# Kernel optimization log

Measured on AMD Instinct MI355X. Metric: run time of the kernel, lower is better.

The kernel has to match this reference:

```python
import jax, jax.numpy as jnp
import numpy as np

EMB = 512
N_ROWS = 10000
N_PAIRS = 65536


def setup_inputs() -> dict:
    key = jax.random.key(0)
    ks = jax.random.split(key, 10)
    s1 = 1.0 / np.sqrt(2 * EMB)
    s2 = 1.0 / np.sqrt(128)
    s3 = 1.0 / np.sqrt(64)
    return {
        "pos_pairs": jax.random.randint(ks[0], (N_PAIRS, 3), 0, N_ROWS, dtype=jnp.int32),
        "neg_pairs": jax.random.randint(ks[1], (N_PAIRS, 3), 0, N_ROWS, dtype=jnp.int32),
        "drug_embedding": jax.random.normal(ks[2], (N_ROWS, EMB), dtype=jnp.float32),
        "target_embedding": jax.random.normal(ks[3], (N_ROWS, EMB), dtype=jnp.float32),
        "W1": jax.random.normal(ks[4], (2 * EMB, 128), dtype=jnp.float32) * s1,
        "b1": jnp.zeros((128,), dtype=jnp.float32),
        "W2": jax.random.normal(ks[5], (128, 64), dtype=jnp.float32) * s2,
        "b2": jnp.zeros((64,), dtype=jnp.float32),
        "W3": jax.random.normal(ks[6], (64, 1), dtype=jnp.float32) * s3,
        "b3": jnp.zeros((1,), dtype=jnp.float32),
    }


def _mlp(x, W1, b1, W2, b2, W3, b3):
    h = jax.nn.relu(x @ W1 + b1)
    h = jax.nn.relu(h @ W2 + b2)
    return (h @ W3 + b3)[..., 0]  # [N]


def _pair_loss(pairs, drug_emb, tgt_emb, W1, b1, W2, b2, W3, b3):
    d = drug_emb[pairs[:, 0]]            # [N, EMB]
    t1 = tgt_emb[pairs[:, 1]]            # [N, EMB]
    t2 = tgt_emb[pairs[:, 2]]            # [N, EMB]
    a1 = _mlp(jnp.concatenate([d, t1], axis=-1), W1, b1, W2, b2, W3, b3)
    a2 = _mlp(jnp.concatenate([d, t2], axis=-1), W1, b1, W2, b2, W3, b3)
    # per-pair MSE of scalar affinities = (a1 - a2)^2; mean over pairs
    return jnp.mean((a1 - a2) ** 2)


def reference(pos_pairs, neg_pairs, drug_embedding, target_embedding,
              W1, b1, W2, b2, W3, b3):
    pos = _pair_loss(pos_pairs, drug_embedding, target_embedding, W1, b1, W2, b2, W3, b3)
    neg = _pair_loss(neg_pairs, drug_embedding, target_embedding, W1, b1, W2, b2, W3, b3)
    return pos - neg
```

## Files before the change

kernel.cpp:

```cpp
#include <hip/hip_runtime.h>

#define EMB 512
#define NROWS 10000
#define NPAIRS 65536

typedef __bf16 bf16x8 __attribute__((ext_vector_type(8)));
typedef float  f32x4  __attribute__((ext_vector_type(4)));
typedef unsigned int u32x4 __attribute__((ext_vector_type(4)));

__device__ __forceinline__ void split2(float x0, float x1, unsigned* hw, unsigned* lw) {
    unsigned u0 = __float_as_uint(x0), u1 = __float_as_uint(x1);
    unsigned r0 = u0 + 0x7FFFu + ((u0 >> 16) & 1u);
    unsigned r1 = u1 + 0x7FFFu + ((u1 >> 16) & 1u);
    float h0 = __uint_as_float(r0 & 0xFFFF0000u);
    float h1 = __uint_as_float(r1 & 0xFFFF0000u);
    float l0 = x0 - h0, l1 = x1 - h1;
    unsigned v0 = __float_as_uint(l0), v1 = __float_as_uint(l1);
    unsigned s0 = v0 + 0x7FFFu + ((v0 >> 16) & 1u);
    unsigned s1 = v1 + 0x7FFFu + ((v1 >> 16) & 1u);
    *hw = (r0 >> 16) | (r1 & 0xFFFF0000u);
    *lw = (s0 >> 16) | (s1 & 0xFFFF0000u);
}

__global__ __launch_bounds__(256)
void k0_fragment(const float* __restrict__ W1, const float* __restrict__ W2,
                 unsigned short* __restrict__ W1Fhi, unsigned short* __restrict__ W1Flo,
                 unsigned short* __restrict__ W2Fhi, unsigned short* __restrict__ W2Flo)
{
    int e = blockIdx.x * 256 + threadIdx.x;
    float x;
    unsigned short *hp, *lp;
    if (e < 131072) {
        int i  = e & 7;
        int l  = (e >> 3) & 63;
        int nt = (e >> 9) & 7;
        int kt = (e >> 12) & 15;
        int t  = e >> 16;
        int k = kt * 32 + 8 * (l >> 4) + i;
        int n = nt * 16 + (l & 15);
        x = W1[(t * 512 + k) * 128 + n];
        hp = W1Fhi + e; lp = W1Flo + e;
    } else {
        int e2 = e - 131072;
        int i  = e2 & 7;
        int l  = (e2 >> 3) & 63;
        int nt = (e2 >> 9) & 3;
        int kt = e2 >> 11;
        int k = kt * 32 + 8 * (l >> 4) + i;
        int n = nt * 16 + (l & 15);
        x = W2[k * 64 + n];
        hp = W2Fhi + e2; lp = W2Flo + e2;
    }
    unsigned u = __float_as_uint(x);
    unsigned r = u + 0x7FFFu + ((u >> 16) & 1u);
    float hf = __uint_as_float(r & 0xFFFF0000u);
    float lf = x - hf;
    unsigned v = __float_as_uint(lf);
    unsigned s = v + 0x7FFFu + ((v >> 16) & 1u);
    *hp = (unsigned short)(r >> 16);
    *lp = (unsigned short)(s >> 16);
}

#define K1_RT 313

__global__ __launch_bounds__(256)
void k1_mfma(const float* __restrict__ drug, const float* __restrict__ tgt,
             const unsigned* __restrict__ W1Fhi, const unsigned* __restrict__ W1Flo,
             const float* __restrict__ b1,
             float* __restrict__ D, float* __restrict__ T)
{
    __shared__ float Abuf[2][32 * 64];

    int bid = blockIdx.x, tid = threadIdx.x;
    bool isT = bid >= K1_RT;
    int rt = isT ? bid - K1_RT : bid;
    const float* emb = isT ? tgt : drug;
    float* out = isT ? T : D;
    int row0 = rt * 32;

    int wave = tid >> 6, lane = tid & 63;
    int g = lane >> 4, lm = lane & 15;
    int mt = wave & 1, nh = wave >> 1;

    int rr = lane >> 4, cc = lane & 15;
    const float* sp[2];
    #pragma unroll
    for (int it = 0; it < 2; it++) {
        int srow = row0 + wave * 8 + it * 4 + rr;
        if (srow > NROWS - 1) srow = NROWS - 1;
        int schunk = (cc & 8) | ((cc & 7) ^ (srow & 7));
        sp[it] = emb + (size_t)srow * EMB + schunk * 4;
    }

    const u32x4* BH = (const u32x4*)W1Fhi + (isT ? 8192 : 0);
    const u32x4* BL = (const u32x4*)W1Flo + (isT ? 8192 : 0);

    int r = mt * 16 + lm, rs = r & 7;

    f32x4 acc[4];
    #pragma unroll
    for (int j = 0; j < 4; j++) { acc[j][0]=0.f; acc[j][1]=0.f; acc[j][2]=0.f; acc[j][3]=0.f; }

    #pragma unroll
    for (int it = 0; it < 2; it++)
        __builtin_amdgcn_global_load_lds(
            (const __attribute__((address_space(1))) void*)(sp[it]),
            (__attribute__((address_space(3))) void*)((char*)&Abuf[0][0] + wave * 2048 + it * 1024),
            16, 0, 0);

    #pragma unroll
    for (int step = 0; step < 8; step++) {
        int cur = step & 1;
        u32x4 bh[2][4], bl[2][4];
        #pragma unroll
        for (int s = 0; s < 2; s++)
            #pragma unroll
            for (int j = 0; j < 4; j++) {
                int kt32 = step * 2 + s, nt = nh * 4 + j;
                bh[s][j] = BH[(kt32 * 8 + nt) * 64 + lane];
                bl[s][j] = BL[(kt32 * 8 + nt) * 64 + lane];
            }
        if (step < 7) {
            #pragma unroll
            for (int it = 0; it < 2; it++)
                __builtin_amdgcn_global_load_lds(
                    (const __attribute__((address_space(1))) void*)(sp[it] + (step + 1) * 64),
                    (__attribute__((address_space(3))) void*)((char*)&Abuf[cur ^ 1][0] + wave * 2048 + it * 1024),
                    16, 0, 0);
            asm volatile("s_waitcnt vmcnt(2)" ::: "memory");
        } else {
            asm volatile("s_waitcnt vmcnt(0)" ::: "memory");
        }
        __builtin_amdgcn_s_barrier();
        const f32x4* A4 = (const f32x4*)&Abuf[cur][0];
        #pragma unroll
        for (int s = 0; s < 2; s++) {
            f32x4 a0 = A4[r * 16 + s * 8 + ((2 * g) ^ rs)];
            f32x4 a1 = A4[r * 16 + s * 8 + ((2 * g + 1) ^ rs)];
            unsigned h0, h1, h2, h3, l0, l1, l2, l3;
            split2(a0[0], a0[1], &h0, &l0);
            split2(a0[2], a0[3], &h1, &l1);
            split2(a1[0], a1[1], &h2, &l2);
            split2(a1[2], a1[3], &h3, &l3);
            u32x4 ah, al;
            ah[0]=h0; ah[1]=h1; ah[2]=h2; ah[3]=h3;
            al[0]=l0; al[1]=l1; al[2]=l2; al[3]=l3;
            bf16x8 Ah = __builtin_bit_cast(bf16x8, ah);
            bf16x8 Al = __builtin_bit_cast(bf16x8, al);
            #pragma unroll
            for (int j = 0; j < 4; j++) {
                bf16x8 Bh = __builtin_bit_cast(bf16x8, bh[s][j]);
                bf16x8 Bl = __builtin_bit_cast(bf16x8, bl[s][j]);
                acc[j] = __builtin_amdgcn_mfma_f32_16x16x32_bf16(Ah, Bh, acc[j], 0, 0, 0);
                acc[j] = __builtin_amdgcn_mfma_f32_16x16x32_bf16(Ah, Bl, acc[j], 0, 0, 0);
                acc[j] = __builtin_amdgcn_mfma_f32_16x16x32_bf16(Al, Bh, acc[j], 0, 0, 0);
            }
        }
        asm volatile("s_waitcnt lgkmcnt(0)" ::: "memory");
        __builtin_amdgcn_s_barrier();
    }

    #pragma unroll
    for (int j = 0; j < 4; j++) {
        int col = (nh * 4 + j) * 16 + lm;
        float bias = isT ? 0.f : b1[col];
        #pragma unroll
        for (int reg = 0; reg < 4; reg++) {
            int row = row0 + mt * 16 + 4 * g + reg;
            if (row < NROWS) out[row * 128 + col] = acc[j][reg] + bias;
        }
    }
}

__global__ __launch_bounds__(256, 4)
void k2_pairs(const float* __restrict__ D, const float* __restrict__ T,
              const int* __restrict__ pos, const int* __restrict__ neg,
              const unsigned* __restrict__ W2Fhi, const unsigned* __restrict__ W2Flo,
              const float* __restrict__ b2, const float* __restrict__ W3,
              double* __restrict__ partials)
{
    __shared__ float Sbuf[2][96 * 32];
    __shared__ double red[4];

    int tid = threadIdx.x, bid = blockIdx.x;
    int wave = tid >> 6, lane = tid & 63;
    int g = lane >> 4, lm = lane & 15;
    const int* pairs = (bid < 2048) ? pos : neg;
    int p0 = (bid & 2047) * 32;

    int rr = lane >> 3, cc = lane & 7;
    const float* sp[3];
    #pragma unroll
    for (int it = 0; it < 3; it++) {
        int pr = wave * 24 + it * 8 + rr;
        int idxv;
        const float* src;
        if (pr < 32) { idxv = pairs[(p0 + pr) * 3]; src = D; }
        else { int q = pr - 32; idxv = pairs[(p0 + (q >> 1)) * 3 + 1 + (q & 1)]; src = T; }
        sp[it] = src + (size_t)idxv * 128 + ((cc ^ (pr & 7)) << 2);
    }

    const u32x4* BH4 = (const u32x4*)W2Fhi;
    const u32x4* BL4 = (const u32x4*)W2Flo;

    int mt = wave;
    int r = mt * 16 + lm;
    int p = r >> 1;
    int ds = p & 7, ts = r & 7;

    f32x4 acc[4];
    #pragma unroll
    for (int nt = 0; nt < 4; nt++) { acc[nt][0]=0.f; acc[nt][1]=0.f; acc[nt][2]=0.f; acc[nt][3]=0.f; }

    #pragma unroll
    for (int it = 0; it < 3; it++)
        __builtin_amdgcn_global_load_lds(
            (const __attribute__((address_space(1))) void*)(sp[it]),
            (__attribute__((address_space(3))) void*)((char*)&Sbuf[0][0] + wave * 3072 + it * 1024),
            16, 0, 0);

    #pragma unroll
    for (int step = 0; step < 4; step++) {
        int cur = step & 1;
        u32x4 bh[4], bl[4];
        #pragma unroll
        for (int nt = 0; nt < 4; nt++) {
            bh[nt] = BH4[(step * 4 + nt) * 64 + lane];
            bl[nt] = BL4[(step * 4 + nt) * 64 + lane];
        }
        if (step < 3) {
            #pragma unroll
            for (int it = 0; it < 3; it++)
                __builtin_amdgcn_global_load_lds(
                    (const __attribute__((address_space(1))) void*)(sp[it] + (step + 1) * 32),
                    (__attribute__((address_space(3))) void*)((char*)&Sbuf[cur ^ 1][0] + wave * 3072 + it * 1024),
                    16, 0, 0);
            asm volatile("s_waitcnt vmcnt(3)" ::: "memory");
        } else {
            asm volatile("s_waitcnt vmcnt(0)" ::: "memory");
        }
        __builtin_amdgcn_s_barrier();
        const f32x4* dS = (const f32x4*)&Sbuf[cur][0];
        f32x4 d0 = dS[p * 8 + ((2 * g) ^ ds)];
        f32x4 d1 = dS[p * 8 + ((2 * g + 1) ^ ds)];
        f32x4 t0 = dS[(32 + r) * 8 + ((2 * g) ^ ts)];
        f32x4 t1 = dS[(32 + r) * 8 + ((2 * g + 1) ^ ts)];
        float h0 = fmaxf(d0[0] + t0[0], 0.f), h1v = fmaxf(d0[1] + t0[1], 0.f);
        float h2 = fmaxf(d0[2] + t0[2], 0.f), h3 = fmaxf(d0[3] + t0[3], 0.f);
        float h4 = fmaxf(d1[0] + t1[0], 0.f), h5 = fmaxf(d1[1] + t1[1], 0.f);
        float h6 = fmaxf(d1[2] + t1[2], 0.f), h7 = fmaxf(d1[3] + t1[3], 0.f);
        unsigned hq0, hq1, hq2, hq3, lq0, lq1, lq2, lq3;
        split2(h0, h1v, &hq0, &lq0);
        split2(h2, h3,  &hq1, &lq1);
        split2(h4, h5,  &hq2, &lq2);
        split2(h6, h7,  &hq3, &lq3);
        u32x4 ah, al;
        ah[0]=hq0; ah[1]=hq1; ah[2]=hq2; ah[3]=hq3;
        al[0]=lq0; al[1]=lq1; al[2]=lq2; al[3]=lq3;
        bf16x8 Ah = __builtin_bit_cast(bf16x8, ah);
        bf16x8 Al = __builtin_bit_cast(bf16x8, al);
        #pragma unroll
        for (int nt = 0; nt < 4; nt++) {
            bf16x8 Bh = __builtin_bit_cast(bf16x8, bh[nt]);
            bf16x8 Bl = __builtin_bit_cast(bf16x8, bl[nt]);
            acc[nt] = __builtin_amdgcn_mfma_f32_16x16x32_bf16(Ah, Bh, acc[nt], 0, 0, 0);
            acc[nt] = __builtin_amdgcn_mfma_f32_16x16x32_bf16(Ah, Bl, acc[nt], 0, 0, 0);
            acc[nt] = __builtin_amdgcn_mfma_f32_16x16x32_bf16(Al, Bh, acc[nt], 0, 0, 0);
        }
        asm volatile("s_waitcnt lgkmcnt(0)" ::: "memory");
        __builtin_amdgcn_s_barrier();
    }

    float b2v[4], w3v[4];
    #pragma unroll
    for (int nt = 0; nt < 4; nt++) { b2v[nt] = b2[nt * 16 + lm]; w3v[nt] = W3[nt * 16 + lm]; }

    float pr[4];
    #pragma unroll
    for (int reg = 0; reg < 4; reg++) {
        float s = 0.f;
        #pragma unroll
        for (int nt = 0; nt < 4; nt++) {
            float h2 = fmaxf(acc[nt][reg] + b2v[nt], 0.f);
            s = fmaf(h2, w3v[nt], s);
        }
        pr[reg] = s;
    }
    #pragma unroll
    for (int m = 1; m <= 8; m <<= 1)
        #pragma unroll
        for (int reg = 0; reg < 4; reg++)
            pr[reg] += __shfl_xor(pr[reg], m, 64);

    float dd0 = pr[0] - pr[1];
    float dd1 = pr[2] - pr[3];
    double dsq = (double)dd0 * (double)dd0 + (double)dd1 * (double)dd1;
    dsq += __shfl_xor(dsq, 16, 64);
    dsq += __shfl_xor(dsq, 32, 64);

    if (lane == 0) red[wave] = dsq;
    __syncthreads();
    if (tid == 0) partials[bid] = red[0] + red[1] + red[2] + red[3];
}

__global__ __launch_bounds__(256)
void k3_final(const double* __restrict__ partials, float* __restrict__ out)
{
    __shared__ double sred[2][4];
    int t = threadIdx.x;
    double sp = 0.0, sn = 0.0;
    #pragma unroll
    for (int i = 0; i < 8; i++) {
        sp += partials[t + 256 * i];
        sn += partials[2048 + t + 256 * i];
    }
    #pragma unroll
    for (int m = 1; m <= 32; m <<= 1) {
        sp += __shfl_xor(sp, m, 64);
        sn += __shfl_xor(sn, m, 64);
    }
    int wave = t >> 6, lane = t & 63;
    if (lane == 0) { sred[0][wave] = sp; sred[1][wave] = sn; }
    __syncthreads();
    if (t == 0) {
        double SP = sred[0][0] + sred[0][1] + sred[0][2] + sred[0][3];
        double SN = sred[1][0] + sred[1][1] + sred[1][2] + sred[1][3];
        out[0] = (float)((SP - SN) / (double)NPAIRS);
    }
}

extern "C" void kernel_launch(void* const* d_in, const int* in_sizes, int n_in,
                              void* d_out, int out_size, void* d_ws, size_t ws_size,
                              hipStream_t stream) {
    const int*   pos  = (const int*)d_in[0];
    const int*   neg  = (const int*)d_in[1];
    const float* drug = (const float*)d_in[2];
    const float* tgt  = (const float*)d_in[3];
    const float* W1   = (const float*)d_in[4];
    const float* b1   = (const float*)d_in[5];
    const float* W2   = (const float*)d_in[6];
    const float* b2   = (const float*)d_in[7];
    const float* W3   = (const float*)d_in[8];

    float* Dp = (float*)d_ws;
    float* Tp = Dp + NROWS * 128;
    char* base = (char*)(Tp + NROWS * 128);
    unsigned short* W2Fhi = (unsigned short*)base;
    unsigned short* W2Flo = W2Fhi + 8192;
    unsigned short* W1Fhi = W2Flo + 8192;
    unsigned short* W1Flo = W1Fhi + 131072;
    double* partials = (double*)(W1Flo + 131072);
    float* out = (float*)d_out;

    k0_fragment<<<544, 256, 0, stream>>>(W1, W2, W1Fhi, W1Flo, W2Fhi, W2Flo);
    k1_mfma<<<2 * K1_RT, 256, 0, stream>>>(drug, tgt, (const unsigned*)W1Fhi,
                                           (const unsigned*)W1Flo, b1, Dp, Tp);
    k2_pairs<<<4096, 256, 0, stream>>>(Dp, Tp, pos, neg, (const unsigned*)W2Fhi,
                                       (const unsigned*)W2Flo, b2, W3, partials);
    k3_final<<<1, 256, 0, stream>>>(partials, out);
}
```

Baseline: 64.18 us.

## Load full K tile into LDS upfront, drop per-step double-buffer barriers

Both kernels now issue every global-to-LDS load for the whole K dimension at the start (64KB for k1, 48KB for k2), then run one barrier followed by a barrier-free MFMA loop. The aim is to remove the per-step waitcnt/barrier handshakes of the double-buffered pipeline and keep more loads in flight at once. The cost is much larger LDS per block, which lowers occupancy. Any overlap between loading and compute now has to come from other resident blocks. The launch bound hint of 4 blocks on k2 is removed to match.

```diff
diff --git a/kernel.cpp b/kernel.cpp
--- a/kernel.cpp
+++ b/kernel.cpp
@@ -69,7 +69,7 @@
              const float* __restrict__ b1,
              float* __restrict__ D, float* __restrict__ T)
 {
-    __shared__ float Abuf[2][32 * 64];
+    __shared__ float Abuf[32 * 512];
 
     int bid = blockIdx.x, tid = threadIdx.x;
     bool isT = bid >= K1_RT;
@@ -82,82 +82,59 @@
     int g = lane >> 4, lm = lane & 15;
     int mt = wave & 1, nh = wave >> 1;
 
-    int rr = lane >> 4, cc = lane & 15;
-    const float* sp[2];
-    #pragma unroll
-    for (int it = 0; it < 2; it++) {
-        int srow = row0 + wave * 8 + it * 4 + rr;
+    #pragma unroll
+    for (int it = 0; it < 16; it++) {
+        int pr = wave * 8 + (it >> 1);
+        int srow = row0 + pr;
         if (srow > NROWS - 1) srow = NROWS - 1;
-        int schunk = (cc & 8) | ((cc & 7) ^ (srow & 7));
-        sp[it] = emb + (size_t)srow * EMB + schunk * 4;
-    }
+        int c = (it & 1) * 64 + lane;
+        int sc = (c & ~7) | ((lane & 7) ^ (pr & 7));
+        __builtin_amdgcn_global_load_lds(
+            (const __attribute__((address_space(1))) void*)(emb + (size_t)srow * EMB + sc * 4),
+            (__attribute__((address_space(3))) void*)((char*)Abuf + wave * 16384 + it * 1024),
+            16, 0, 0);
+    }
+    __syncthreads();
 
     const u32x4* BH = (const u32x4*)W1Fhi + (isT ? 8192 : 0);
     const u32x4* BL = (const u32x4*)W1Flo + (isT ? 8192 : 0);
-
-    int r = mt * 16 + lm, rs = r & 7;
+    const f32x4* A4 = (const f32x4*)Abuf;
+
+    int r = mt * 16 + lm, rk = r & 7;
 
     f32x4 acc[4];
     #pragma unroll
     for (int j = 0; j < 4; j++) { acc[j][0]=0.f; acc[j][1]=0.f; acc[j][2]=0.f; acc[j][3]=0.f; }
 
-    #pragma unroll
-    for (int it = 0; it < 2; it++)
-        __builtin_amdgcn_global_load_lds(
-            (const __attribute__((address_space(1))) void*)(sp[it]),
-            (__attribute__((address_space(3))) void*)((char*)&Abuf[0][0] + wave * 2048 + it * 1024),
-            16, 0, 0);
-
-    #pragma unroll
-    for (int step = 0; step < 8; step++) {
-        int cur = step & 1;
-        u32x4 bh[2][4], bl[2][4];
-        #pragma unroll
-        for (int s = 0; s < 2; s++)
-            #pragma unroll
-            for (int j = 0; j < 4; j++) {
-                int kt32 = step * 2 + s, nt = nh * 4 + j;
-                bh[s][j] = BH[(kt32 * 8 + nt) * 64 + lane];
-                bl[s][j] = BL[(kt32 * 8 + nt) * 64 + lane];
-            }
-        if (step < 7) {
-            #pragma unroll
-            for (int it = 0; it < 2; it++)
-                __builtin_amdgcn_global_load_lds(
-                    (const __attribute__((address_space(1))) void*)(sp[it] + (step + 1) * 64),
-                    (__attribute__((address_space(3))) void*)((char*)&Abuf[cur ^ 1][0] + wave * 2048 + it * 1024),
-                    16, 0, 0);
-            asm volatile("s_waitcnt vmcnt(2)" ::: "memory");
-        } else {
-            asm volatile("s_waitcnt vmcnt(0)" ::: "memory");
-        }
-        __builtin_amdgcn_s_barrier();
-        const f32x4* A4 = (const f32x4*)&Abuf[cur][0];
-        #pragma unroll
-        for (int s = 0; s < 2; s++) {
-            f32x4 a0 = A4[r * 16 + s * 8 + ((2 * g) ^ rs)];
-            f32x4 a1 = A4[r * 16 + s * 8 + ((2 * g + 1) ^ rs)];
-            unsigned h0, h1, h2, h3, l0, l1, l2, l3;
-            split2(a0[0], a0[1], &h0, &l0);
-            split2(a0[2], a0[3], &h1, &l1);
-            split2(a1[0], a1[1], &h2, &l2);
-            split2(a1[2], a1[3], &h3, &l3);
-            u32x4 ah, al;
-            ah[0]=h0; ah[1]=h1; ah[2]=h2; ah[3]=h3;
-            al[0]=l0; al[1]=l1; al[2]=l2; al[3]=l3;
-            bf16x8 Ah = __builtin_bit_cast(bf16x8, ah);
-            bf16x8 Al = __builtin_bit_cast(bf16x8, al);
-            #pragma unroll
-            for (int j = 0; j < 4; j++) {
-                bf16x8 Bh = __builtin_bit_cast(bf16x8, bh[s][j]);
-                bf16x8 Bl = __builtin_bit_cast(bf16x8, bl[s][j]);
-                acc[j] = __builtin_amdgcn_mfma_f32_16x16x32_bf16(Ah, Bh, acc[j], 0, 0, 0);
-                acc[j] = __builtin_amdgcn_mfma_f32_16x16x32_bf16(Ah, Bl, acc[j], 0, 0, 0);
-                acc[j] = __builtin_amdgcn_mfma_f32_16x16x32_bf16(Al, Bh, acc[j], 0, 0, 0);
-            }
-        }
-        asm volatile("s_waitcnt lgkmcnt(0)" ::: "memory");
-        __builtin_amdgcn_s_barrier();
+    #pragma unroll 4
+    for (int kt = 0; kt < 16; kt++) {
+        u32x4 bh[4], bl[4];
+        #pragma unroll
+        for (int j = 0; j < 4; j++) {
+            int nt = nh * 4 + j;
+            bh[j] = BH[(kt * 8 + nt) * 64 + lane];
+            bl[j] = BL[(kt * 8 + nt) * 64 + lane];
+        }
+        f32x4 a0 = A4[r * 128 + kt * 8 + ((2 * g)     ^ rk)];
+        f32x4 a1 = A4[r * 128 + kt * 8 + ((2 * g + 1) ^ rk)];
+        unsigned h0, h1, h2, h3, l0, l1, l2, l3;
+        split2(a0[0], a0[1], &h0, &l0);
+        split2(a0[2], a0[3], &h1, &l1);
+        split2(a1[0], a1[1], &h2, &l2);
+        split2(a1[2], a1[3], &h3, &l3);
+        u32x4 ah, al;
+        ah[0]=h0; ah[1]=h1; ah[2]=h2; ah[3]=h3;
+        al[0]=l0; al[1]=l1; al[2]=l2; al[3]=l3;
+        bf16x8 Ah = __builtin_bit_cast(bf16x8, ah);
+        bf16x8 Al = __builtin_bit_cast(bf16x8, al);
+        #pragma unroll
+        for (int j = 0; j < 4; j++) {
+            bf16x8 Bh = __builtin_bit_cast(bf16x8, bh[j]);
+            bf16x8 Bl = __builtin_bit_cast(bf16x8, bl[j]);
+            acc[j] = __builtin_amdgcn_mfma_f32_16x16x32_bf16(Ah, Bh, acc[j], 0, 0, 0);
+            acc[j] = __builtin_amdgcn_mfma_f32_16x16x32_bf16(Ah, Bl, acc[j], 0, 0, 0);
+            acc[j] = __builtin_amdgcn_mfma_f32_16x16x32_bf16(Al, Bh, acc[j], 0, 0, 0);
+        }
     }
 
     #pragma unroll
@@ -172,14 +149,14 @@
     }
 }
 
-__global__ __launch_bounds__(256, 4)
+__global__ __launch_bounds__(256)
 void k2_pairs(const float* __restrict__ D, const float* __restrict__ T,
               const int* __restrict__ pos, const int* __restrict__ neg,
               const unsigned* __restrict__ W2Fhi, const unsigned* __restrict__ W2Flo,
               const float* __restrict__ b2, const float* __restrict__ W3,
               double* __restrict__ partials)
 {
-    __shared__ float Sbuf[2][96 * 32];
+    __shared__ float Sbuf[96 * 128];
     __shared__ double red[4];
 
     int tid = threadIdx.x, bid = blockIdx.x;
@@ -188,63 +165,46 @@
     const int* pairs = (bid < 2048) ? pos : neg;
     int p0 = (bid & 2047) * 32;
 
-    int rr = lane >> 3, cc = lane & 7;
-    const float* sp[3];
-    #pragma unroll
-    for (int it = 0; it < 3; it++) {
-        int pr = wave * 24 + it * 8 + rr;
+    #pragma unroll
+    for (int it = 0; it < 12; it++) {
+        int pr = wave * 24 + it * 2 + (lane >> 5);
         int idxv;
         const float* src;
         if (pr < 32) { idxv = pairs[(p0 + pr) * 3]; src = D; }
         else { int q = pr - 32; idxv = pairs[(p0 + (q >> 1)) * 3 + 1 + (q & 1)]; src = T; }
-        sp[it] = src + (size_t)idxv * 128 + ((cc ^ (pr & 7)) << 2);
-    }
+        int c = lane & 31;
+        int sc = (c & 24) | ((c & 7) ^ (pr & 7));
+        __builtin_amdgcn_global_load_lds(
+            (const __attribute__((address_space(1))) void*)(src + (size_t)idxv * 128 + sc * 4),
+            (__attribute__((address_space(3))) void*)((char*)Sbuf + wave * 12288 + it * 1024),
+            16, 0, 0);
+    }
+    __syncthreads();
 
     const u32x4* BH4 = (const u32x4*)W2Fhi;
     const u32x4* BL4 = (const u32x4*)W2Flo;
-
-    int mt = wave;
-    int r = mt * 16 + lm;
+    const f32x4* S4 = (const f32x4*)Sbuf;
+
+    int r = wave * 16 + lm;
     int p = r >> 1;
-    int ds = p & 7, ts = r & 7;
+    int pk = p & 7, tk = r & 7;
 
     f32x4 acc[4];
     #pragma unroll
     for (int nt = 0; nt < 4; nt++) { acc[nt][0]=0.f; acc[nt][1]=0.f; acc[nt][2]=0.f; acc[nt][3]=0.f; }
 
     #pragma unroll
-    for (int it = 0; it < 3; it++)
-        __builtin_amdgcn_global_load_lds(
-            (const __attribute__((address_space(1))) void*)(sp[it]),
-            (__attribute__((address_space(3))) void*)((char*)&Sbuf[0][0] + wave * 3072 + it * 1024),
-            16, 0, 0);
-
-    #pragma unroll
     for (int step = 0; step < 4; step++) {
-        int cur = step & 1;
         u32x4 bh[4], bl[4];
         #pragma unroll
         for (int nt = 0; nt < 4; nt++) {
             bh[nt] = BH4[(step * 4 + nt) * 64 + lane];
             bl[nt] = BL4[(step * 4 + nt) * 64 + lane];
         }
-        if (step < 3) {
-            #pragma unroll
-            for (int it = 0; it < 3; it++)
-                __builtin_amdgcn_global_load_lds(
-                    (const __attribute__((address_space(1))) void*)(sp[it] + (step + 1) * 32),
-                    (__attribute__((address_space(3))) void*)((char*)&Sbuf[cur ^ 1][0] + wave * 3072 + it * 1024),
-                    16, 0, 0);
-            asm volatile("s_waitcnt vmcnt(3)" ::: "memory");
-        } else {
-            asm volatile("s_waitcnt vmcnt(0)" ::: "memory");
-        }
-        __builtin_amdgcn_s_barrier();
-        const f32x4* dS = (const f32x4*)&Sbuf[cur][0];
-        f32x4 d0 = dS[p * 8 + ((2 * g) ^ ds)];
-        f32x4 d1 = dS[p * 8 + ((2 * g + 1) ^ ds)];
-        f32x4 t0 = dS[(32 + r) * 8 + ((2 * g) ^ ts)];
-        f32x4 t1 = dS[(32 + r) * 8 + ((2 * g + 1) ^ ts)];
+        f32x4 d0 = S4[p * 32 + step * 8 + ((2 * g)     ^ pk)];
+        f32x4 d1 = S4[p * 32 + step * 8 + ((2 * g + 1) ^ pk)];
+        f32x4 t0 = S4[(32 + r) * 32 + step * 8 + ((2 * g)     ^ tk)];
+        f32x4 t1 = S4[(32 + r) * 32 + step * 8 + ((2 * g + 1) ^ tk)];
         float h0 = fmaxf(d0[0] + t0[0], 0.f), h1v = fmaxf(d0[1] + t0[1], 0.f);
         float h2 = fmaxf(d0[2] + t0[2], 0.f), h3 = fmaxf(d0[3] + t0[3], 0.f);
         float h4 = fmaxf(d1[0] + t1[0], 0.f), h5 = fmaxf(d1[1] + t1[1], 0.f);
@@ -267,8 +227,6 @@
             acc[nt] = __builtin_amdgcn_mfma_f32_16x16x32_bf16(Ah, Bl, acc[nt], 0, 0, 0);
             acc[nt] = __builtin_amdgcn_mfma_f32_16x16x32_bf16(Al, Bh, acc[nt], 0, 0, 0);
         }
-        asm volatile("s_waitcnt lgkmcnt(0)" ::: "memory");
-        __builtin_amdgcn_s_barrier();
     }
 
     float b2v[4], w3v[4];
```

New measurement: 90.57 us. +41.1%, slower.
